# Performance work log

Hardware: AMD Instinct MI355X
Metric: run time of the kernel (lower is better)

## Reference

```python
import jax, jax.numpy as jnp
import numpy as np

AN = 1.0      # bandwidth a_n
SIGMA = 1.0   # Gaussian kernel scale
_EPS = 1e-32


def setup_inputs() -> dict:
    key = jax.random.key(0)
    k1, k2, k3 = jax.random.split(key, 3)
    n = 8192
    log_h = jax.random.normal(k1, (n, 1), dtype=jnp.float32)
    durations = jax.random.uniform(k2, (n,), dtype=jnp.float32)
    events = jax.random.randint(k3, (n,), 0, 2, dtype=jnp.int32)
    return {"log_h": log_h, "durations": durations, "events": events}


def reference(log_h, durations, events):
    theta = log_h.reshape(-1)                         # (n,)
    n = theta.shape[0]
    # residuals e = -(theta - log(Y)); note original adds 1e-32 before log
    e = -(theta - jnp.log(durations + _EPS))          # (n,)
    perm = jnp.argsort(e)                             # sort order of e
    e_sorted = e[perm]                                # (n,) ascending
    # Original code sorts [indices, dur, ev, theta] by the indices column,
    # which reorders the side arrays by the INVERSE permutation.
    inv = jnp.argsort(perm)
    ev = events.astype(jnp.float32)[inv]              # (n,)
    th = theta[inv]                                   # (n,)

    diff = (e_sorted[:, None] - e_sorted[None, :]) / AN   # (n, n)
    # Normal(0, SIGMA) log pdf at diff
    log_pdf = -0.5 * (diff / SIGMA) ** 2 - jnp.log(SIGMA * jnp.sqrt(2.0 * jnp.pi))
    # cond_E_i = sum_j pdf_ij * ev_j / (n*an) + eps-per-element
    cond_E = jnp.sum(jnp.exp(log_pdf) * ev / (n * AN) + _EPS, axis=1)   # (n,)
    # Normal(0, SIGMA) cdf at diff
    cdf = 0.5 * (1.0 + jax.lax.erf(diff / (SIGMA * jnp.sqrt(2.0))))
    surv = jnp.sum(cdf / n, axis=1)                   # (n,)

    loss = -jnp.sum((jnp.log(cond_E) - jnp.log(surv) + th) * ev / n)
    return loss
```

## Files before the change

### kernel.cpp

```cpp
#include <hip/hip_runtime.h>
#include <math.h>
#include <stdint.h>

#define RB 256
#define JT 512
#define GM 1024
#define YS 128

#define SCALE 0.84932180028801904f
#define SQRT2PI 2.5066282746310002f
#define KFP 0.46971863934f
#define LN2 0.69314718056f

__device__ __forceinline__ uint64_t order_key(float f, int idx) {
  unsigned u = __float_as_uint(f);
  u = (u & 0x80000000u) ? ~u : (u | 0x80000000u);
  return ((uint64_t)u << 32) | (unsigned)idx;
}

__device__ __forceinline__ float e_of(const float* theta, const float* dur, int i) {
  return logf(dur[i] + 1e-32f) - theta[i];
}

__device__ __forceinline__ void grid_geom(const float2* xe, int n, float* x0, float* hx) {
  float a = xe[0].x - 7.0f;
  float b = xe[n - 1].x + 7.0f;
  *x0 = a;
  *hx = (b - a) / (float)(GM - 1);
}

__global__ __launch_bounds__(RB) void rank_part_kernel(
    const float* __restrict__ theta, const float* __restrict__ dur,
    int* __restrict__ rank_part, int n) {
  __shared__ uint64_t kt[JT];
  const int i = blockIdx.x * RB + threadIdx.x;
  uint64_t ki = order_key(e_of(theta, dur, i), i);
  const int jbase = blockIdx.y * JT;
  for (int t = threadIdx.x; t < JT; t += RB) {
    int j = jbase + t;
    kt[t] = order_key(e_of(theta, dur, j), j);
  }
  __syncthreads();
  int cnt = 0;
  #pragma unroll 8
  for (int jj = 0; jj < JT; ++jj) cnt += (kt[jj] < ki) ? 1 : 0;
  rank_part[blockIdx.y * n + i] = cnt;
}

__global__ __launch_bounds__(RB) void scatter_kernel(
    const float* __restrict__ theta, const float* __restrict__ dur,
    const int* __restrict__ ev, const int* __restrict__ rank_part,
    float2* __restrict__ xe, float* __restrict__ th_s,
    float* __restrict__ gbuf, float* __restrict__ out, int n) {
  int k = blockIdx.x * RB + threadIdx.x;
  int r = 0;
  const int nj = n / JT;
  #pragma unroll 16
  for (int jch = 0; jch < nj; ++jch) r += rank_part[jch * n + k];
  ((float*)&xe[r])[0] = SCALE * e_of(theta, dur, k);
  ((float*)&xe[k])[1] = (float)ev[r];
  th_s[k] = theta[r];
  if (k < 4 * GM) gbuf[k] = 0.0f;
  if (k == 0) out[0] = 0.0f;
}

__global__ __launch_bounds__(RB) void gt_kernel(
    const float2* __restrict__ xe, float* __restrict__ gbuf, int n) {
  float x0, hx;
  grid_geom(xe, n, &x0, &hx);
  int m = blockIdx.x * RB + threadIdx.x;
  float xm = fmaf((float)m, hx, x0);
  const int chunk = n / YS;
  int jb = blockIdx.y * chunk;
  const float P2S = 0.39169197f;
  float a = 0.0f, b = 0.0f, f = 0.0f, d = 0.0f;
  #pragma unroll 8
  for (int jj = 0; jj < chunk; ++jj) {
    float2 q = xe[jb + jj];
    float dp = xm - q.x;
    float g = __builtin_amdgcn_exp2f(-(dp * dp));
    float evg = q.y * g;
    a += g;
    b += evg;
    d = fmaf(dp, evg, d);
    float tt = __builtin_amdgcn_rcpf(fmaf(P2S, __builtin_fabsf(dp), 1.0f));
    float poly = tt * (0.3480242f + tt * (-0.0958798f + tt * 0.7478556f));
    f += __builtin_copysignf(fmaf(-poly, g, 1.0f), dp);
  }
  atomicAdd(&gbuf[m], a);
  atomicAdd(&gbuf[GM + m], b);
  atomicAdd(&gbuf[2 * GM + m], 0.5f * (float)chunk + 0.5f * f);
  atomicAdd(&gbuf[3 * GM + m], d);
}

__global__ __launch_bounds__(RB) void final_kernel(
    const float2* __restrict__ xe, const float* __restrict__ th_s,
    const float* __restrict__ gbuf, float* __restrict__ out, int n) {
  float x0, hx;
  grid_geom(xe, n, &x0, &hx);
  const float* A = gbuf;
  const float* B = gbuf + GM;
  const float* F = gbuf + 2 * GM;
  const float* D = gbuf + 3 * GM;
  int i = blockIdx.x * RB + threadIdx.x;

  float term = 0.0f;
  if (i < n) {
    float2 q = xe[i];
    float u = (q.x - x0) * __builtin_amdgcn_rcpf(hx);
    int m = (int)u;
    m = min(max(m, 0), GM - 2);
    float t = u - (float)m;
    t = fminf(fmaxf(t, 0.0f), 1.0f);
    float t2 = t * t, t3 = t2 * t;
    float h00 = 2.0f * t3 - 3.0f * t2 + 1.0f;
    float h01 = 3.0f * t2 - 2.0f * t3;
    float h10 = t3 - 2.0f * t2 + t;
    float h11 = t3 - t2;
    float Fi = F[m] * h00 + F[m + 1] * h01 +
               hx * KFP * (A[m] * h10 + A[m + 1] * h11);
    float Bi = B[m] * h00 + B[m + 1] * h01 -
               2.0f * LN2 * hx * (D[m] * h10 + D[m + 1] * h11);
    const float fn = (float)n;
    float condE = fmaxf(Bi, 0.0f) * (1.0f / SQRT2PI) / fn + fn * 1e-32f;
    float surv = fmaxf(Fi, 0.25f) / fn;
    term = (__logf(condE) - __logf(surv) + th_s[i]) * q.y;
  }

  #pragma unroll
  for (int off = 32; off > 0; off >>= 1) term += __shfl_down(term, off, 64);
  __shared__ float red[RB / 64];
  int wave = threadIdx.x >> 6, lane = threadIdx.x & 63;
  if (lane == 0) red[wave] = term;
  __syncthreads();
  if (threadIdx.x == 0) {
    float s = 0.0f;
    #pragma unroll
    for (int w = 0; w < RB / 64; ++w) s += red[w];
    atomicAdd(out, -s / (float)n);
  }
}

extern "C" void kernel_launch(void* const* d_in, const int* in_sizes, int n_in,
                              void* d_out, int out_size, void* d_ws, size_t ws_size,
                              hipStream_t stream) {
  const float* theta = (const float*)d_in[0];
  const float* dur   = (const float*)d_in[1];
  const int*   ev    = (const int*)d_in[2];
  float* out = (float*)d_out;
  const int n = in_sizes[1];

  char* ws = (char*)d_ws;
  float2* xe        = (float2*)ws;  ws += n * sizeof(float2);
  int*    rank_part = (int*)ws;     ws += (n / JT) * n * sizeof(int);
  float*  th_s      = (float*)ws;   ws += n * sizeof(float);
  float*  gbuf      = (float*)ws;   ws += 4 * GM * sizeof(float);

  rank_part_kernel<<<dim3(n / RB, n / JT), RB, 0, stream>>>(theta, dur, rank_part, n);
  scatter_kernel<<<n / RB, RB, 0, stream>>>(theta, dur, ev, rank_part,
                                            xe, th_s, gbuf, out, n);
  gt_kernel<<<dim3(GM / RB, YS), RB, 0, stream>>>(xe, gbuf, n);
  final_kernel<<<n / RB, RB, 0, stream>>>(xe, th_s, gbuf, out, n);
}
```

Measured before the change: 77.67 us.

## Fuse four kernels into one cooperative kernel with grid-wide syncs

```diff
diff --git a/kernel.cpp b/kernel.cpp
--- a/kernel.cpp
+++ b/kernel.cpp
@@ -1,11 +1,16 @@
 #include <hip/hip_runtime.h>
+#include <hip/hip_cooperative_groups.h>
 #include <math.h>
 #include <stdint.h>
 
+namespace cg = cooperative_groups;
+
 #define RB 256
-#define JT 512
+#define BLKS 512
+#define JT 128
+#define IPT 4
 #define GM 1024
-#define YS 128
+#define CH 64
 
 #define SCALE 0.84932180028801904f
 #define SQRT2PI 2.5066282746310002f
@@ -29,115 +34,145 @@
   *hx = (b - a) / (float)(GM - 1);
 }
 
-__global__ __launch_bounds__(RB) void rank_part_kernel(
+__global__ __launch_bounds__(RB, 2) void fused_kernel(
     const float* __restrict__ theta, const float* __restrict__ dur,
-    int* __restrict__ rank_part, int n) {
-  __shared__ uint64_t kt[JT];
-  const int i = blockIdx.x * RB + threadIdx.x;
-  uint64_t ki = order_key(e_of(theta, dur, i), i);
-  const int jbase = blockIdx.y * JT;
-  for (int t = threadIdx.x; t < JT; t += RB) {
-    int j = jbase + t;
-    kt[t] = order_key(e_of(theta, dur, j), j);
-  }
-  __syncthreads();
-  int cnt = 0;
-  #pragma unroll 8
-  for (int jj = 0; jj < JT; ++jj) cnt += (kt[jj] < ki) ? 1 : 0;
-  rank_part[blockIdx.y * n + i] = cnt;
-}
-
-__global__ __launch_bounds__(RB) void scatter_kernel(
-    const float* __restrict__ theta, const float* __restrict__ dur,
-    const int* __restrict__ ev, const int* __restrict__ rank_part,
+    const int* __restrict__ ev, int* __restrict__ rank_part,
     float2* __restrict__ xe, float* __restrict__ th_s,
     float* __restrict__ gbuf, float* __restrict__ out, int n) {
-  int k = blockIdx.x * RB + threadIdx.x;
-  int r = 0;
-  const int nj = n / JT;
-  #pragma unroll 16
-  for (int jch = 0; jch < nj; ++jch) r += rank_part[jch * n + k];
-  ((float*)&xe[r])[0] = SCALE * e_of(theta, dur, k);
-  ((float*)&xe[k])[1] = (float)ev[r];
-  th_s[k] = theta[r];
-  if (k < 4 * GM) gbuf[k] = 0.0f;
-  if (k == 0) out[0] = 0.0f;
-}
+  cg::grid_group grid = cg::this_grid();
+  __shared__ uint64_t kt[JT];
+  __shared__ float2 cst[CH];
+  __shared__ float red[RB / 64];
 
-__global__ __launch_bounds__(RB) void gt_kernel(
-    const float2* __restrict__ xe, float* __restrict__ gbuf, int n) {
-  float x0, hx;
-  grid_geom(xe, n, &x0, &hx);
-  int m = blockIdx.x * RB + threadIdx.x;
-  float xm = fmaf((float)m, hx, x0);
-  const int chunk = n / YS;
-  int jb = blockIdx.y * chunk;
-  const float P2S = 0.39169197f;
-  float a = 0.0f, b = 0.0f, f = 0.0f, d = 0.0f;
-  #pragma unroll 8
-  for (int jj = 0; jj < chunk; ++jj) {
-    float2 q = xe[jb + jj];
-    float dp = xm - q.x;
-    float g = __builtin_amdgcn_exp2f(-(dp * dp));
-    float evg = q.y * g;
-    a += g;
-    b += evg;
-    d = fmaf(dp, evg, d);
-    float tt = __builtin_amdgcn_rcpf(fmaf(P2S, __builtin_fabsf(dp), 1.0f));
-    float poly = tt * (0.3480242f + tt * (-0.0958798f + tt * 0.7478556f));
-    f += __builtin_copysignf(fmaf(-poly, g, 1.0f), dp);
-  }
-  atomicAdd(&gbuf[m], a);
-  atomicAdd(&gbuf[GM + m], b);
-  atomicAdd(&gbuf[2 * GM + m], 0.5f * (float)chunk + 0.5f * f);
-  atomicAdd(&gbuf[3 * GM + m], d);
-}
+  const int tid = threadIdx.x;
+  const int bid = blockIdx.x;
 
-__global__ __launch_bounds__(RB) void final_kernel(
-    const float2* __restrict__ xe, const float* __restrict__ th_s,
-    const float* __restrict__ gbuf, float* __restrict__ out, int n) {
-  float x0, hx;
-  grid_geom(xe, n, &x0, &hx);
-  const float* A = gbuf;
-  const float* B = gbuf + GM;
-  const float* F = gbuf + 2 * GM;
-  const float* D = gbuf + 3 * GM;
-  int i = blockIdx.x * RB + threadIdx.x;
-
-  float term = 0.0f;
-  if (i < n) {
-    float2 q = xe[i];
-    float u = (q.x - x0) * __builtin_amdgcn_rcpf(hx);
-    int m = (int)u;
-    m = min(max(m, 0), GM - 2);
-    float t = u - (float)m;
-    t = fminf(fmaxf(t, 0.0f), 1.0f);
-    float t2 = t * t, t3 = t2 * t;
-    float h00 = 2.0f * t3 - 3.0f * t2 + 1.0f;
-    float h01 = 3.0f * t2 - 2.0f * t3;
-    float h10 = t3 - 2.0f * t2 + t;
-    float h11 = t3 - t2;
-    float Fi = F[m] * h00 + F[m + 1] * h01 +
-               hx * KFP * (A[m] * h10 + A[m + 1] * h11);
-    float Bi = B[m] * h00 + B[m + 1] * h01 -
-               2.0f * LN2 * hx * (D[m] * h10 + D[m + 1] * h11);
-    const float fn = (float)n;
-    float condE = fmaxf(Bi, 0.0f) * (1.0f / SQRT2PI) / fn + fn * 1e-32f;
-    float surv = fmaxf(Fi, 0.25f) / fn;
-    term = (__logf(condE) - __logf(surv) + th_s[i]) * q.y;
+  {
+    const int bx = bid & 7;
+    const int by = bid >> 3;
+    const int i0 = bx * (RB * IPT) + tid;
+    uint64_t ki[IPT];
+    #pragma unroll
+    for (int p = 0; p < IPT; ++p) {
+      int ii = i0 + p * RB;
+      ki[p] = order_key(e_of(theta, dur, ii), ii);
+    }
+    if (tid < JT) {
+      int j = by * JT + tid;
+      kt[tid] = order_key(e_of(theta, dur, j), j);
+    }
+    __syncthreads();
+    int cnt[IPT] = {0, 0, 0, 0};
+    const ulonglong2* kt2 = (const ulonglong2*)kt;
+    #pragma unroll 8
+    for (int jj = 0; jj < JT / 2; ++jj) {
+      ulonglong2 q = kt2[jj];
+      #pragma unroll
+      for (int p = 0; p < IPT; ++p) {
+        cnt[p] += (q.x < ki[p]) ? 1 : 0;
+        cnt[p] += (q.y < ki[p]) ? 1 : 0;
+      }
+    }
+    #pragma unroll
+    for (int p = 0; p < IPT; ++p)
+      rank_part[by * n + i0 + p * RB] = cnt[p];
   }
 
-  #pragma unroll
-  for (int off = 32; off > 0; off >>= 1) term += __shfl_down(term, off, 64);
-  __shared__ float red[RB / 64];
-  int wave = threadIdx.x >> 6, lane = threadIdx.x & 63;
-  if (lane == 0) red[wave] = term;
-  __syncthreads();
-  if (threadIdx.x == 0) {
-    float s = 0.0f;
-    #pragma unroll
-    for (int w = 0; w < RB / 64; ++w) s += red[w];
-    atomicAdd(out, -s / (float)n);
+  grid.sync();
+
+  {
+    int k = bid * RB + tid;
+    if (k < n) {
+      int r = 0;
+      #pragma unroll 16
+      for (int jch = 0; jch < 64; ++jch) r += rank_part[jch * n + k];
+      ((float*)&xe[r])[0] = SCALE * e_of(theta, dur, k);
+      ((float*)&xe[k])[1] = (float)ev[r];
+      th_s[k] = theta[r];
+    }
+    int k2 = k - n;
+    if (k2 >= 0 && k2 < 4 * GM) gbuf[k2] = 0.0f;
+    if (k == n) out[0] = 0.0f;
+  }
+
+  grid.sync();
+
+  {
+    float x0, hx;
+    grid_geom(xe, n, &x0, &hx);
+    int m = (bid & 3) * RB + tid;
+    float xm = fmaf((float)m, hx, x0);
+    int jb = (bid >> 2) * CH;
+    if (tid < CH) cst[tid] = xe[jb + tid];
+    __syncthreads();
+    const float P2S = 0.39169197f;
+    float a = 0.0f, b = 0.0f, f = 0.0f, d = 0.0f;
+    #pragma unroll 8
+    for (int jj = 0; jj < CH; ++jj) {
+      float2 q = cst[jj];
+      float dp = xm - q.x;
+      float g = __builtin_amdgcn_exp2f(-(dp * dp));
+      float evg = q.y * g;
+      a += g;
+      b += evg;
+      d = fmaf(dp, evg, d);
+      float tt = __builtin_amdgcn_rcpf(fmaf(P2S, __builtin_fabsf(dp), 1.0f));
+      float poly = tt * (0.3480242f + tt * (-0.0958798f + tt * 0.7478556f));
+      f += __builtin_copysignf(fmaf(-poly, g, 1.0f), dp);
+    }
+    atomicAdd(&gbuf[m], a);
+    atomicAdd(&gbuf[GM + m], b);
+    atomicAdd(&gbuf[2 * GM + m], 0.5f * (float)CH + 0.5f * f);
+    atomicAdd(&gbuf[3 * GM + m], d);
+  }
+
+  grid.sync();
+
+  {
+    float x0, hx;
+    grid_geom(xe, n, &x0, &hx);
+    const float* A = gbuf;
+    const float* B = gbuf + GM;
+    const float* F = gbuf + 2 * GM;
+    const float* D = gbuf + 3 * GM;
+    int i = bid * RB + tid;
+
+    float term = 0.0f;
+    if (i < n) {
+      float2 q = xe[i];
+      float u = (q.x - x0) * __builtin_amdgcn_rcpf(hx);
+      int m = (int)u;
+      m = min(max(m, 0), GM - 2);
+      float t = u - (float)m;
+      t = fminf(fmaxf(t, 0.0f), 1.0f);
+      float t2 = t * t, t3 = t2 * t;
+      float h00 = 2.0f * t3 - 3.0f * t2 + 1.0f;
+      float h01 = 3.0f * t2 - 2.0f * t3;
+      float h10 = t3 - 2.0f * t2 + t;
+      float h11 = t3 - t2;
+      float Fi = F[m] * h00 + F[m + 1] * h01 +
+                 hx * KFP * (A[m] * h10 + A[m + 1] * h11);
+      float Bi = B[m] * h00 + B[m + 1] * h01 -
+                 2.0f * LN2 * hx * (D[m] * h10 + D[m + 1] * h11);
+      const float fn = (float)n;
+      float condE = fmaxf(Bi, 0.0f) * (1.0f / SQRT2PI) / fn + fn * 1e-32f;
+      float surv = fmaxf(Fi, 0.25f) / fn;
+      term = (__logf(condE) - __logf(surv) + th_s[i]) * q.y;
+    }
+
+    if (bid < n / RB) {
+      #pragma unroll
+      for (int off = 32; off > 0; off >>= 1) term += __shfl_down(term, off, 64);
+      int wave = tid >> 6, lane = tid & 63;
+      if (lane == 0) red[wave] = term;
+      __syncthreads();
+      if (tid == 0) {
+        float s = 0.0f;
+        #pragma unroll
+        for (int w = 0; w < RB / 64; ++w) s += red[w];
+        atomicAdd(out, -s / (float)n);
+      }
+    }
   }
 }
 
@@ -148,7 +183,7 @@
   const float* dur   = (const float*)d_in[1];
   const int*   ev    = (const int*)d_in[2];
   float* out = (float*)d_out;
-  const int n = in_sizes[1];
+  int n = in_sizes[1];
 
   char* ws = (char*)d_ws;
   float2* xe        = (float2*)ws;  ws += n * sizeof(float2);
@@ -156,9 +191,8 @@
   float*  th_s      = (float*)ws;   ws += n * sizeof(float);
   float*  gbuf      = (float*)ws;   ws += 4 * GM * sizeof(float);
 
-  rank_part_kernel<<<dim3(n / RB, n / JT), RB, 0, stream>>>(theta, dur, rank_part, n);
-  scatter_kernel<<<n / RB, RB, 0, stream>>>(theta, dur, ev, rank_part,
-                                            xe, th_s, gbuf, out, n);
-  gt_kernel<<<dim3(GM / RB, YS), RB, 0, stream>>>(xe, gbuf, n);
-  final_kernel<<<n / RB, RB, 0, stream>>>(xe, th_s, gbuf, out, n);
+  void* args[] = {(void*)&theta, (void*)&dur, (void*)&ev, (void*)&rank_part,
+                  (void*)&xe, (void*)&th_s, (void*)&gbuf, (void*)&out, (void*)&n};
+  hipLaunchCooperativeKernel((const void*)fused_kernel, dim3(BLKS), dim3(RB),
+                             args, 0, stream);
 }
```

After: 224.5 us. +189.0%, slower.
